# Performance work log

Hardware: AMD Instinct MI355X
Metric: run time of the kernel (lower is better)

Reference implementation:

```python
import jax, jax.numpy as jnp
import numpy as np

N_NODES = 100000


def _gcn_conv(x, edge_index, W, b):
    # edge_index: [2, E] (src, dst). PyG GCNConv: add self-loops, symmetric norm.
    n = x.shape[0]
    src = jnp.concatenate([edge_index[0], jnp.arange(n, dtype=edge_index.dtype)])
    dst = jnp.concatenate([edge_index[1], jnp.arange(n, dtype=edge_index.dtype)])
    deg = jax.ops.segment_sum(jnp.ones_like(dst, dtype=x.dtype), dst, num_segments=n)
    dinv = jnp.where(deg > 0, jax.lax.rsqrt(deg), 0.0)
    norm = dinv[src] * dinv[dst]                      # [E+N]
    h = x @ W                                         # transform first (small dim)
    msg = h[src] * norm[:, None]                      # gather + normalize
    out = jax.ops.segment_sum(msg, dst, num_segments=n)  # scatter-aggregate
    return out + b


def setup_inputs() -> dict:
    key = jax.random.key(0)
    ks = jax.random.split(key, 8)
    x = jax.random.normal(ks[0], (N_NODES, 128), dtype=jnp.float32)
    edge_index = jax.random.randint(ks[1], (2, 1600000), 0, N_NODES, dtype=jnp.int32)
    def glorot(k, shape):
        lim = float(np.sqrt(6.0 / (shape[0] + shape[1])))
        return jax.random.uniform(k, shape, jnp.float32, -lim, lim)
    return {
        "x": x,
        "edge_index": edge_index,
        "W1": glorot(ks[2], (128, 64)),
        "b1": jnp.zeros((64,), jnp.float32),
        "W2": glorot(ks[3], (64, 64)),
        "b2": jnp.zeros((64,), jnp.float32),
        "Wh": glorot(ks[4], (64, 40)),
        "bh": jnp.zeros((40,), jnp.float32),
    }


def reference(x, edge_index, W1, b1, W2, b2, Wh, bh):
    # eval mode: dropout is identity
    h = jax.nn.relu(_gcn_conv(x, edge_index, W1, b1))
    h = jax.nn.relu(_gcn_conv(h, edge_index, W2, b2))
    return h @ Wh + bh  # [N, num_classes]
```

## Files before the change

### kernel.cpp

```cpp
#include <hip/hip_runtime.h>
#include <hip/hip_bf16.h>


#define BIN_SHIFT 9
#define BN        (1 << BIN_SHIFT)
#define NB_MAX    256
#define BIN_CHUNK 4096

__device__ __forceinline__ float bf2f(unsigned short u) {
  union { unsigned i; float f; } c; c.i = ((unsigned)u) << 16; return c.f;
}
__device__ __forceinline__ unsigned short f2bf(float f) {
  union { float f; unsigned i; } c; c.f = f;
  unsigned r = c.i + 0x7FFFu + ((c.i >> 16) & 1u);
  return (unsigned short)(r >> 16);
}

__global__ __launch_bounds__(256) void k_zero(int* p, int n) {
  int i = blockIdx.x * blockDim.x + threadIdx.x;
  if (i < n) p[i] = 0;
}

__global__ __launch_bounds__(64) void k_zrow(unsigned short* hs, int n) {
  if (threadIdx.x < 32) ((unsigned*)(hs + (size_t)n * 64))[threadIdx.x] = 0u;
}

__global__ __launch_bounds__(256) void k_bhist(const int* __restrict__ dst,
                                               int* bhist, int E, int nb) {
  __shared__ int lh[NB_MAX];
  lh[threadIdx.x] = 0;
  __syncthreads();
  for (int i = blockIdx.x * 256 + threadIdx.x; i < E; i += gridDim.x * 256)
    atomicAdd(&lh[dst[i] >> BIN_SHIFT], 1);
  __syncthreads();
  int v = lh[threadIdx.x];
  if (threadIdx.x < nb && v) atomicAdd(&bhist[threadIdx.x], v);
}

__global__ __launch_bounds__(256) void k_bscan(const int* __restrict__ bhist,
                                               int* boff, int* gcur, int nb, int E) {
  __shared__ int sh[256];
  const int t = threadIdx.x;
  int v = (t < nb) ? bhist[t] : 0;
  sh[t] = v;
  __syncthreads();
  for (int d = 1; d < 256; d <<= 1) {
    int x = (t >= d) ? sh[t - d] : 0;
    __syncthreads();
    sh[t] += x;
    __syncthreads();
  }
  if (t < nb) { int e = sh[t] - v; boff[t] = e; gcur[t] = e; }
  if (t == 0) boff[nb] = E;
}

__global__ __launch_bounds__(256) void k_bin(
    const int* __restrict__ src, const int* __restrict__ dst,
    int* gcur, int* __restrict__ binned, int E)
{
  __shared__ int  hist[NB_MAX];
  __shared__ int  excl[NB_MAX];
  __shared__ int  lcur[NB_MAX];
  __shared__ int  gbase[NB_MAX];
  __shared__ int2 stage[BIN_CHUNK];

  const int t = threadIdx.x;
  const int base = blockIdx.x * BIN_CHUNK;
  const int m = min(BIN_CHUNK, E - base);

  int2 pr[BIN_CHUNK / 256];
  int nmine = 0;
  #pragma unroll
  for (int i = 0; i < BIN_CHUNK / 256; ++i) {
    int idx = t + 256 * i;
    if (idx < m) {
      pr[i].x = src[base + idx];
      pr[i].y = dst[base + idx];
      nmine = i + 1;
    }
  }

  hist[t] = 0;
  __syncthreads();
  #pragma unroll
  for (int i = 0; i < BIN_CHUNK / 256; ++i)
    if (i < nmine) atomicAdd(&hist[pr[i].y >> BIN_SHIFT], 1);
  __syncthreads();

  const int mycnt = hist[t];
  for (int d = 1; d < 256; d <<= 1) {
    int v = (t >= d) ? hist[t - d] : 0;
    __syncthreads();
    hist[t] += v;
    __syncthreads();
  }
  {
    int e = hist[t] - mycnt;
    excl[t] = e;
    lcur[t] = e;
    gbase[t] = mycnt ? atomicAdd(&gcur[t], mycnt) : 0;
  }
  __syncthreads();

  #pragma unroll
  for (int i = 0; i < BIN_CHUNK / 256; ++i)
    if (i < nmine) {
      int b = pr[i].y >> BIN_SHIFT;
      int p = atomicAdd(&lcur[b], 1);
      stage[p] = pr[i];
    }
  __syncthreads();

  for (int i = t; i < m; i += 256) {
    int2 pp = stage[i];
    int b = pp.y >> BIN_SHIFT;
    binned[gbase[b] + (i - excl[b])] =
        (pp.x << BIN_SHIFT) | (pp.y & (BN - 1));
  }
}

__global__ __launch_bounds__(256) void k_csr(
    const int* __restrict__ binned, const int* __restrict__ boff,
    int* __restrict__ offs, int* __restrict__ endo,
    float* __restrict__ dinv, int* __restrict__ csr, int n)
{
  __shared__ int cnt_l[BN];
  __shared__ int tsum[256];
  __shared__ int lcur[BN];
  const int t = threadIdx.x;
  const int b = blockIdx.x;
  const int base = boff[b];
  const int end  = boff[b + 1];
  const int n0 = b << BIN_SHIFT;

  cnt_l[t] = 0; cnt_l[t + 256] = 0;
  __syncthreads();
  for (int i = base + t; i < end; i += 256)
    atomicAdd(&cnt_l[binned[i] & (BN - 1)], 1);
  __syncthreads();

  const int c0 = cnt_l[2 * t];
  const int c1 = cnt_l[2 * t + 1];
  const int s = c0 + c1;
  tsum[t] = s;
  __syncthreads();
  for (int d = 1; d < 256; d <<= 1) {
    int v = (t >= d) ? tsum[t - d] : 0;
    __syncthreads();
    tsum[t] += v;
    __syncthreads();
  }
  const int ex = tsum[t] - s;
  const int e0 = ex, e1 = ex + c0;
  const int g0 = n0 + 2 * t, g1 = g0 + 1;
  if (g0 < n) {
    offs[g0] = base + e0; endo[g0] = base + e1;
    dinv[g0] = rsqrtf((float)(c0 + 1));
  }
  if (g1 < n) {
    offs[g1] = base + e1; endo[g1] = base + e1 + c1;
    dinv[g1] = rsqrtf((float)(c1 + 1));
  }
  lcur[2 * t] = e0;
  lcur[2 * t + 1] = e1;
  __syncthreads();
  for (int i = base + t; i < end; i += 256) {
    int v = binned[i];
    int p = atomicAdd(&lcur[v & (BN - 1)], 1);
    csr[base + p] = v >> BIN_SHIFT;
  }
}

__global__ __launch_bounds__(256) void k_count(const int* __restrict__ dst, int* cnt, int E) {
  int e = blockIdx.x * blockDim.x + threadIdx.x;
  if (e < E) atomicAdd(&cnt[dst[e]], 1);
}
__global__ __launch_bounds__(256) void k_dinv(const int* __restrict__ cnt, float* dinv, int n) {
  int i = blockIdx.x * blockDim.x + threadIdx.x;
  if (i < n) dinv[i] = rsqrtf((float)(cnt[i] + 1));
}
__global__ __launch_bounds__(256) void k_scan1(const int* __restrict__ cnt,
                                               int* offs, int* bsum, int n) {
  __shared__ int sh[256];
  const int t = threadIdx.x;
  const int base = blockIdx.x * 1024 + t * 4;
  int v0 = 0, v1 = 0, v2 = 0, v3 = 0;
  if (base + 0 < n) v0 = cnt[base + 0];
  if (base + 1 < n) v1 = cnt[base + 1];
  if (base + 2 < n) v2 = cnt[base + 2];
  if (base + 3 < n) v3 = cnt[base + 3];
  const int s = v0 + v1 + v2 + v3;
  sh[t] = s;
  __syncthreads();
  for (int d = 1; d < 256; d <<= 1) {
    int x = (t >= d) ? sh[t - d] : 0;
    __syncthreads();
    sh[t] += x;
    __syncthreads();
  }
  int o = sh[t] - s;
  if (t == 255) bsum[blockIdx.x] = sh[255];
  if (base + 0 < n) { offs[base + 0] = o; o += v0; }
  if (base + 1 < n) { offs[base + 1] = o; o += v1; }
  if (base + 2 < n) { offs[base + 2] = o; o += v2; }
  if (base + 3 < n) { offs[base + 3] = o; o += v3; }
}
__global__ __launch_bounds__(256) void k_scan2(int* bsum, int nb) {
  __shared__ int sh[256];
  const int t = threadIdx.x;
  int v = (t < nb) ? bsum[t] : 0;
  sh[t] = v;
  __syncthreads();
  for (int d = 1; d < 256; d <<= 1) {
    int x = (t >= d) ? sh[t - d] : 0;
    __syncthreads();
    sh[t] += x;
    __syncthreads();
  }
  if (t < nb) bsum[t] = sh[t] - v;
}
__global__ __launch_bounds__(256) void k_scan3(int* offs, const int* __restrict__ bsum,
                                               int* cursor, int n) {
  int i = blockIdx.x * blockDim.x + threadIdx.x;
  if (i < n) {
    int o = offs[i] + bsum[i >> 10];
    offs[i] = o;
    cursor[i] = o;
  }
}
__global__ __launch_bounds__(256) void k_fill(const int* __restrict__ src,
                                              const int* __restrict__ dst,
                                              int* cursor, int* csr, int E) {
  int e = blockIdx.x * blockDim.x + threadIdx.x;
  if (e < E) {
    int p = atomicAdd(&cursor[dst[e]], 1);
    csr[p] = src[e];
  }
}

template<int K, int NOUT, bool SCALE, bool BIAS, bool OUTBF>
__global__ __launch_bounds__(256) void k_gemm(
    const float* __restrict__ X, const float* __restrict__ W,
    const float* __restrict__ dinv, const float* __restrict__ bias,
    void* __restrict__ Yv, int nrows)
{
  constexpr int LDX = 68;
  constexpr int LDW = K + 4;
  constexpr int NC  = (NOUT + 15) / 16;
  __shared__ float Xs[64 * LDX];
  __shared__ float WT[NC * 16 * LDW];

  const int t  = threadIdx.x;
  const int tx = t & 15;
  const int ty = t >> 4;
  const int r0 = blockIdx.x * 64;

  for (int idx = t; idx < K * NOUT; idx += 256) {
    int k = idx / NOUT, col = idx - k * NOUT;
    WT[col * LDW + k] = W[idx];
  }

  float acc[4][NC];
  #pragma unroll
  for (int i = 0; i < 4; ++i)
    #pragma unroll
    for (int j = 0; j < NC; ++j) acc[i][j] = 0.f;

  for (int kt = 0; kt < K; kt += 64) {
    __syncthreads();
    #pragma unroll
    for (int it = 0; it < 4; ++it) {
      int f4  = it * 256 + t;
      int row = f4 >> 4;
      int kk  = (f4 & 15) * 4;
      int gr  = r0 + row; if (gr >= nrows) gr = nrows - 1;
      *(float4*)&Xs[row * LDX + kk] = *(const float4*)&X[(size_t)gr * K + kt + kk];
    }
    __syncthreads();

    #pragma unroll 4
    for (int k = 0; k < 64; k += 4) {
      float4 xv[4], wv[NC];
      #pragma unroll
      for (int i = 0; i < 4; ++i)
        xv[i] = *(const float4*)&Xs[(ty * 4 + i) * LDX + k];
      #pragma unroll
      for (int j = 0; j < NC; ++j)
        wv[j] = *(const float4*)&WT[(tx + 16 * j) * LDW + kt + k];
      #pragma unroll
      for (int i = 0; i < 4; ++i)
        #pragma unroll
        for (int j = 0; j < NC; ++j) {
          acc[i][j] = fmaf(xv[i].x, wv[j].x, acc[i][j]);
          acc[i][j] = fmaf(xv[i].y, wv[j].y, acc[i][j]);
          acc[i][j] = fmaf(xv[i].z, wv[j].z, acc[i][j]);
          acc[i][j] = fmaf(xv[i].w, wv[j].w, acc[i][j]);
        }
    }
  }

  #pragma unroll
  for (int i = 0; i < 4; ++i) {
    const int row = r0 + ty * 4 + i;
    if (row >= nrows) continue;
    const float sc = SCALE ? dinv[row] : 1.f;
    #pragma unroll
    for (int j = 0; j < NC; ++j) {
      const int col = tx + 16 * j;
      if (col < NOUT) {
        float v = acc[i][j];
        if constexpr (SCALE) v *= sc;
        if constexpr (BIAS)  v += bias[col];
        if constexpr (OUTBF)
          ((unsigned short*)Yv)[(size_t)row * NOUT + col] = f2bf(v);
        else
          ((float*)Yv)[(size_t)row * NOUT + col] = v;
      }
    }
  }
}

__global__ __launch_bounds__(256) void k_pull(
    const unsigned short* __restrict__ hs, const int* __restrict__ csr,
    const int* __restrict__ offs, const int* __restrict__ endo,
    const float* __restrict__ dinv, const float* __restrict__ bias,
    float* __restrict__ out, int n)
{
  const int node = blockIdx.x * 4 + (threadIdx.x >> 6);
  if (node >= n) return;
  const int lane = threadIdx.x & 63;
  const int g    = lane >> 4;
  const int fl   = lane & 15;

  const int beg = offs[node];
  const int m   = endo[node] - beg;
  const int mp  = (m + 3) & ~3;

  float a0 = 0.f, a1 = 0.f, a2 = 0.f, a3 = 0.f;

  for (int base = 0; base < mp; base += 64) {
    const int rem = mp - base;
    const int kk  = rem < 64 ? rem : 64;
    const int myidx = (base + lane < m) ? csr[beg + base + lane] : n;
    const int nq = kk >> 2;
    #pragma unroll 4
    for (int i = 0; i < nq; ++i) {
      int s = __shfl(myidx, 4 * i + g);
      uint2 u = *(const uint2*)&hs[(size_t)s * 64 + fl * 4];
      a0 += bf2f((unsigned short)u.x); a1 += bf2f((unsigned short)(u.x >> 16));
      a2 += bf2f((unsigned short)u.y); a3 += bf2f((unsigned short)(u.y >> 16));
    }
  }

  a0 += __shfl_xor(a0, 16); a1 += __shfl_xor(a1, 16);
  a2 += __shfl_xor(a2, 16); a3 += __shfl_xor(a3, 16);
  a0 += __shfl_xor(a0, 32); a1 += __shfl_xor(a1, 32);
  a2 += __shfl_xor(a2, 32); a3 += __shfl_xor(a3, 32);

  if (lane < 16) {
    uint2 u = *(const uint2*)&hs[(size_t)node * 64 + fl * 4];
    a0 += bf2f((unsigned short)u.x); a1 += bf2f((unsigned short)(u.x >> 16));
    a2 += bf2f((unsigned short)u.y); a3 += bf2f((unsigned short)(u.y >> 16));
    const float dv = dinv[node];
    const float4 bb = *(const float4*)&bias[fl * 4];
    float4 o;
    o.x = fmaxf(fmaf(dv, a0, bb.x), 0.f);
    o.y = fmaxf(fmaf(dv, a1, bb.y), 0.f);
    o.z = fmaxf(fmaf(dv, a2, bb.z), 0.f);
    o.w = fmaxf(fmaf(dv, a3, bb.w), 0.f);
    *(float4*)&out[(size_t)node * 64 + fl * 4] = o;
  }
}

extern "C" void kernel_launch(void* const* d_in, const int* in_sizes, int n_in,
                              void* d_out, int out_size, void* d_ws, size_t ws_size,
                              hipStream_t stream) {
  const float* x  = (const float*)d_in[0];
  const int*   ei = (const int*)d_in[1];
  const float* W1 = (const float*)d_in[2];
  const float* b1 = (const float*)d_in[3];
  const float* W2 = (const float*)d_in[4];
  const float* b2 = (const float*)d_in[5];
  const float* Wh = (const float*)d_in[6];
  const float* bh = (const float*)d_in[7];
  float* out = (float*)d_out;

  const int N = in_sizes[0] / 128;
  const int E = in_sizes[1] / 2;
  const int* src = ei;
  const int* dst = ei + E;

  auto align_up = [](size_t v, size_t a) { return (v + a - 1) & ~(a - 1); };
  char* ws = (char*)d_ws;
  size_t off = 0;
  int*   cnt    = (int*)(ws + off);   off = align_up(off + (size_t)N * 4, 256);
  float* dinv   = (float*)(ws + off); off = align_up(off + (size_t)N * 4, 256);
  int*   offs   = (int*)(ws + off);   off = align_up(off + (size_t)N * 4, 256);
  int*   endo   = (int*)(ws + off);   off = align_up(off + (size_t)N * 4, 256);
  int*   bsum   = (int*)(ws + off);   off = align_up(off + 256 * 4, 256);
  int*   bhist  = (int*)(ws + off);   off = align_up(off + NB_MAX * 4, 256);
  int*   boff   = (int*)(ws + off);   off = align_up(off + (NB_MAX + 1) * 4, 256);
  int*   gcur   = (int*)(ws + off);   off = align_up(off + NB_MAX * 4, 256);
  int*   csr    = (int*)(ws + off);   off = align_up(off + (size_t)E * 4, 256);
  int*   binned = (int*)(ws + off);   off = align_up(off + (size_t)E * 4, 256);
  unsigned short* A = (unsigned short*)(ws + off);
  off = align_up(off + (size_t)(N + 1) * 64 * 2, 256);
  float* B      = (float*)(ws + off); off = align_up(off + (size_t)N * 64 * 4, 256);
  (void)ws_size;

  const int TB = 256;
  const int gN = (N + TB - 1) / TB;
  const int gE = (E + TB - 1) / TB;
  const int NBk = (N + BN - 1) >> BIN_SHIFT;
  const int gGemm = (N + 63) / 64;
  const int gPull = (N + 3) / 4;
  const int gBin  = (E + BIN_CHUNK - 1) / BIN_CHUNK;

  k_zrow<<<1, 64, 0, stream>>>(A, N);

  if (NBk <= NB_MAX) {
    k_zero <<<1, TB, 0, stream>>>(bhist, NBk);
    k_bhist<<<512, TB, 0, stream>>>(dst, bhist, E, NBk);
    k_bscan<<<1, TB, 0, stream>>>(bhist, boff, gcur, NBk, E);
    k_bin  <<<gBin, TB, 0, stream>>>(src, dst, gcur, binned, E);
    k_csr  <<<NBk, TB, 0, stream>>>(binned, boff, offs, endo, dinv, csr, N);
  } else {
    k_zero <<<gN, TB, 0, stream>>>(cnt, N);
    k_count<<<gE, TB, 0, stream>>>(dst, cnt, E);
    k_dinv <<<gN, TB, 0, stream>>>(cnt, dinv, N);
    const int nb1 = (N + 1023) / 1024;
    k_scan1<<<nb1, TB, 0, stream>>>(cnt, offs, bsum, N);
    k_scan2<<<1,  TB, 0, stream>>>(bsum, nb1);
    k_scan3<<<gN, TB, 0, stream>>>(offs, bsum, endo, N);
    k_fill <<<gE, TB, 0, stream>>>(src, dst, endo, csr, E);
  }

  k_gemm<128, 64, true, false, true><<<gGemm, TB, 0, stream>>>(x, W1, dinv, nullptr, A, N);
  k_pull<<<gPull, TB, 0, stream>>>(A, csr, offs, endo, dinv, b1, B, N);

  k_gemm<64, 64, true, false, true><<<gGemm, TB, 0, stream>>>(B, W2, dinv, nullptr, A, N);
  k_pull<<<gPull, TB, 0, stream>>>(A, csr, offs, endo, dinv, b2, B, N);

  k_gemm<64, 40, false, true, false><<<gGemm, TB, 0, stream>>>(B, Wh, nullptr, bh, out, N);
}
```

Measured before the change: 240.1 us.

## Use bf16 MFMA with swizzled LDS tiles in dense GEMM kernel

Replaces the scalar fp32 FMA register-tiled GEMM with bf16 MFMA 16x16x32 instructions. X and W are converted to bf16 when loaded into LDS, and the LDS layout uses an XOR swizzle to avoid bank conflicts. Each wave computes a 16-row strip across all output columns. This cuts ALU time in the feature transforms but lowers the precision of the GEMM inputs to bf16.

```diff
diff --git a/kernel.cpp b/kernel.cpp
--- a/kernel.cpp
+++ b/kernel.cpp
@@ -6,6 +6,9 @@
 #define BN        (1 << BIN_SHIFT)
 #define NB_MAX    256
 #define BIN_CHUNK 4096
+
+typedef __attribute__((ext_vector_type(8))) short short8v;
+typedef __attribute__((ext_vector_type(4))) float f32x4;
 
 __device__ __forceinline__ float bf2f(unsigned short u) {
   union { unsigned i; float f; } c; c.i = ((unsigned)u) << 16; return c.f;
@@ -244,71 +247,68 @@
     const float* __restrict__ dinv, const float* __restrict__ bias,
     void* __restrict__ Yv, int nrows)
 {
-  constexpr int LDX = 68;
-  constexpr int LDW = K + 4;
-  constexpr int NC  = (NOUT + 15) / 16;
-  __shared__ float Xs[64 * LDX];
-  __shared__ float WT[NC * 16 * LDW];
-
-  const int t  = threadIdx.x;
-  const int tx = t & 15;
-  const int ty = t >> 4;
+  constexpr int NCOL = (NOUT + 15) & ~15;
+  constexpr int NT   = NCOL / 16;
+  constexpr int KS   = K / 32;
+  __shared__ __align__(16) unsigned short Xs[64 * K];
+  __shared__ __align__(16) unsigned short WTs[NCOL * K];
+
+  const int t = threadIdx.x;
   const int r0 = blockIdx.x * 64;
 
+  if constexpr (NCOL != NOUT) {
+    for (int i = t; i < (NCOL - NOUT) * K; i += 256)
+      WTs[NOUT * K + i] = 0;
+  }
   for (int idx = t; idx < K * NOUT; idx += 256) {
-    int k = idx / NOUT, col = idx - k * NOUT;
-    WT[col * LDW + k] = W[idx];
-  }
-
-  float acc[4][NC];
-  #pragma unroll
-  for (int i = 0; i < 4; ++i)
+    int k = idx / NOUT, n = idx - k * NOUT;
+    int u = (k >> 3) ^ (n & 7);
+    WTs[n * K + u * 8 + (k & 7)] = f2bf(W[idx]);
+  }
+  for (int q = t; q < 16 * K; q += 256) {
+    int row = q / (K / 4);
+    int c4  = q - row * (K / 4);
+    int gr  = r0 + row; if (gr >= nrows) gr = nrows - 1;
+    float4 v = *(const float4*)&X[(size_t)gr * K + c4 * 4];
+    int u = (c4 >> 1) ^ (row & 7);
+    unsigned short* p = &Xs[row * K + u * 8 + (c4 & 1) * 4];
+    p[0] = f2bf(v.x); p[1] = f2bf(v.y); p[2] = f2bf(v.z); p[3] = f2bf(v.w);
+  }
+  __syncthreads();
+
+  const int wid  = t >> 6;
+  const int lane = t & 63;
+  const int l15  = lane & 15;
+  const int kb   = lane >> 4;
+  const int lrow = 16 * wid + l15;
+
+  f32x4 acc[NT];
+  #pragma unroll
+  for (int j = 0; j < NT; ++j) { f32x4 z = {0.f, 0.f, 0.f, 0.f}; acc[j] = z; }
+
+  #pragma unroll
+  for (int ks = 0; ks < KS; ++ks) {
+    const int ub = ks * 4 + kb;
+    short8v a = *(const short8v*)&Xs[lrow * K + (ub ^ (lrow & 7)) * 8];
     #pragma unroll
-    for (int j = 0; j < NC; ++j) acc[i][j] = 0.f;
-
-  for (int kt = 0; kt < K; kt += 64) {
-    __syncthreads();
-    #pragma unroll
-    for (int it = 0; it < 4; ++it) {
-      int f4  = it * 256 + t;
-      int row = f4 >> 4;
-      int kk  = (f4 & 15) * 4;
-      int gr  = r0 + row; if (gr >= nrows) gr = nrows - 1;
-      *(float4*)&Xs[row * LDX + kk] = *(const float4*)&X[(size_t)gr * K + kt + kk];
+    for (int j = 0; j < NT; ++j) {
+      const int n = j * 16 + l15;
+      short8v b = *(const short8v*)&WTs[n * K + (ub ^ (n & 7)) * 8];
+      acc[j] = __builtin_amdgcn_mfma_f32_16x16x32_bf16(a, b, acc[j], 0, 0, 0);
     }
-    __syncthreads();
-
-    #pragma unroll 4
-    for (int k = 0; k < 64; k += 4) {
-      float4 xv[4], wv[NC];
-      #pragma unroll
-      for (int i = 0; i < 4; ++i)
-        xv[i] = *(const float4*)&Xs[(ty * 4 + i) * LDX + k];
-      #pragma unroll
-      for (int j = 0; j < NC; ++j)
-        wv[j] = *(const float4*)&WT[(tx + 16 * j) * LDW + kt + k];
-      #pragma unroll
-      for (int i = 0; i < 4; ++i)
-        #pragma unroll
-        for (int j = 0; j < NC; ++j) {
-          acc[i][j] = fmaf(xv[i].x, wv[j].x, acc[i][j]);
-          acc[i][j] = fmaf(xv[i].y, wv[j].y, acc[i][j]);
-          acc[i][j] = fmaf(xv[i].z, wv[j].z, acc[i][j]);
-          acc[i][j] = fmaf(xv[i].w, wv[j].w, acc[i][j]);
-        }
-    }
-  }
-
-  #pragma unroll
-  for (int i = 0; i < 4; ++i) {
-    const int row = r0 + ty * 4 + i;
+  }
+
+  const int rbase = r0 + 16 * wid + kb * 4;
+  #pragma unroll
+  for (int r = 0; r < 4; ++r) {
+    const int row = rbase + r;
     if (row >= nrows) continue;
     const float sc = SCALE ? dinv[row] : 1.f;
     #pragma unroll
-    for (int j = 0; j < NC; ++j) {
-      const int col = tx + 16 * j;
+    for (int j = 0; j < NT; ++j) {
+      const int col = j * 16 + l15;
       if (col < NOUT) {
-        float v = acc[i][j];
+        float v = acc[j][r];
         if constexpr (SCALE) v *= sc;
         if constexpr (BIAS)  v += bias[col];
         if constexpr (OUTBF)
```

Result: faster. 204.6 us (-14.8%).
